# Performance work log

Measured on AMD Instinct MI355X. Metric: run time of the kernel, lower is better.

Reference implementation:

```python
import jax, jax.numpy as jnp
import numpy as np

D_MODEL = 1024
N_HEAD = 16
POWER = 4
EPS = 1e-6
MASK_FILL = -1000.0


def setup_inputs() -> dict:
    key = jax.random.key(0)
    ks = jax.random.split(key, 10)
    B, T, C = 2, 2048, D_MODEL
    sc = 1.0 / np.sqrt(C)
    inp = {
        "x": jax.random.normal(ks[0], (B, T, C), jnp.float32),
        "Wq": jax.random.normal(ks[1], (C, C), jnp.float32) * sc,
        "bq": jnp.zeros((C,), jnp.float32),
        "Wk": jax.random.normal(ks[2], (C, C), jnp.float32) * sc,
        "bk": jnp.zeros((C,), jnp.float32),
        "Wv": jax.random.normal(ks[3], (C, C), jnp.float32) * sc,
        "bv": jnp.zeros((C,), jnp.float32),
        "Wo": jax.random.normal(ks[4], (C, C), jnp.float32) * sc,
        "bo": jnp.zeros((C,), jnp.float32),
        "score_gain": jnp.asarray(4.0, jnp.float32),
        # True above the diagonal -> masked (causal)
        "causal_mask": jnp.triu(jnp.ones((T, T), jnp.bool_), k=1),
    }
    return inp


def rational_softmax(x):
    s = x / (jnp.abs(x) + 1.0)          # squash to (-1, 1)
    p = ((s + 1.0) * 0.5) ** POWER      # (0,1) then sharpen
    return p / (jnp.sum(p, axis=-1, keepdims=True) + EPS)


def reference(x, Wq, bq, Wk, bk, Wv, bv, Wo, bo, score_gain, causal_mask):
    B, T, C = x.shape
    H, D = N_HEAD, C // N_HEAD
    q = (x @ Wq + bq).reshape(B, T, H, D)
    k = (x @ Wk + bk).reshape(B, T, H, D)
    v = (x @ Wv + bv).reshape(B, T, H, D)
    # scores: (B, H, T, T)
    scores = jnp.einsum('bqhd,bkhd->bhqk', q, k)
    scores = scores - jnp.mean(scores, axis=-1, keepdims=True)
    mad = jnp.mean(jnp.abs(scores), axis=-1, keepdims=True) + 1e-6
    scores = scores / mad * score_gain
    scores = jnp.where(causal_mask, MASK_FILL, scores)
    attn = rational_softmax(scores)
    out = jnp.einsum('bhqk,bkhd->bqhd', attn, v).reshape(B, T, C)
    return out @ Wo + bo
```

## Files before the change

kernel.cpp:

```cpp
#include <hip/hip_runtime.h>
#include <hip/hip_bf16.h>
#include <cstdint>

#define BDIM 2
#define TSEQ 2048
#define CDIM 1024
#define NH 16
#define HD 64
#define NTOK (BDIM*TSEQ)
#define MASK_FILL_V (-1000.0f)
#define EPS_V (1e-6f)

typedef short bf16x8 __attribute__((ext_vector_type(8)));
typedef float f32x4  __attribute__((ext_vector_type(4)));

__device__ __forceinline__ float bf2f(unsigned short u) {
    union { unsigned int i; float f; } x; x.i = ((unsigned int)u) << 16; return x.f;
}
__device__ __forceinline__ unsigned short f2bf(float v) {
    __hip_bfloat16 h = __float2bfloat16(v);
    union { __hip_bfloat16 h; unsigned short u; } c; c.h = h; return c.u;
}
__device__ __forceinline__ float unpk_lo(unsigned int u) {
    union { unsigned int i; float f; } x; x.i = u << 16; return x.f;
}
__device__ __forceinline__ float unpk_hi(unsigned int u) {
    union { unsigned int i; float f; } x; x.i = u & 0xFFFF0000u; return x.f;
}
__device__ __forceinline__ unsigned int pk2(float lo, float hi) {
    unsigned int r;
    asm("v_cvt_pk_bf16_f32 %0, %1, %2" : "=v"(r) : "v"(lo), "v"(hi));
    return r;
}

__device__ __forceinline__ bool dt_is_bf16(const void* gain_p) {
    return ((*(const unsigned int*)gain_p) & 0xFFFFu) == 0x4080u;
}
__device__ __forceinline__ float ld1(const void* p, size_t i, bool bf) {
    return bf ? bf2f(((const unsigned short*)p)[i]) : ((const float*)p)[i];
}

__device__ __forceinline__ void gl2lds16(const unsigned short* g, unsigned short* l) {
    __builtin_amdgcn_global_load_lds(
        (const __attribute__((address_space(1))) unsigned int*)g,
        (__attribute__((address_space(3))) unsigned int*)l, 16, 0, 0);
}

__global__ __launch_bounds__(256) void pack_x_kernel(
    const void* __restrict__ X, const void* __restrict__ gain_p,
    unsigned short* __restrict__ Xb)
{
    const bool bf = dt_is_bf16(gain_p);
    size_t i = ((size_t)blockIdx.x * 256 + threadIdx.x) * 8;
    if (bf) {
        *(bf16x8*)&Xb[i] = *(const bf16x8*)((const unsigned short*)X + i);
    } else {
        const float* xf = (const float*)X;
        float4 a = *(const float4*)&xf[i];
        float4 b = *(const float4*)&xf[i + 4];
        bf16x8 o;
        o[0]=(short)f2bf(a.x); o[1]=(short)f2bf(a.y); o[2]=(short)f2bf(a.z); o[3]=(short)f2bf(a.w);
        o[4]=(short)f2bf(b.x); o[5]=(short)f2bf(b.y); o[6]=(short)f2bf(b.z); o[7]=(short)f2bf(b.w);
        *(bf16x8*)&Xb[i] = o;
    }
}

__global__ __launch_bounds__(256) void pack_wt_kernel(
    const void* __restrict__ Wq, const void* __restrict__ Wk,
    const void* __restrict__ Wv, const void* __restrict__ Wo,
    const void* __restrict__ gain_p, unsigned short* __restrict__ Wt)
{
    __shared__ __align__(16) unsigned short tile[64][72];
    const bool bf = dt_is_bf16(gain_p);
    const int which = blockIdx.z;
    const void* W = (which == 0) ? Wq : (which == 1) ? Wk : (which == 2) ? Wv : Wo;
    const int k0 = blockIdx.y * 64, n0 = blockIdx.x * 64;
    const int t = threadIdx.x;
    const int r = t >> 2, cb = (t & 3) * 16;
    if (bf) {
        const unsigned short* wsd = (const unsigned short*)W;
        *(bf16x8*)&tile[r][cb]     = *(const bf16x8*)&wsd[(size_t)(k0 + r) * CDIM + n0 + cb];
        *(bf16x8*)&tile[r][cb + 8] = *(const bf16x8*)&wsd[(size_t)(k0 + r) * CDIM + n0 + cb + 8];
    } else {
        const float* wf = (const float*)W;
        const float* src = &wf[(size_t)(k0 + r) * CDIM + n0 + cb];
        float4 f0 = *(const float4*)&src[0];
        float4 f1 = *(const float4*)&src[4];
        float4 f2 = *(const float4*)&src[8];
        float4 f3 = *(const float4*)&src[12];
        bf16x8 o0, o1;
        o0[0]=(short)f2bf(f0.x); o0[1]=(short)f2bf(f0.y); o0[2]=(short)f2bf(f0.z); o0[3]=(short)f2bf(f0.w);
        o0[4]=(short)f2bf(f1.x); o0[5]=(short)f2bf(f1.y); o0[6]=(short)f2bf(f1.z); o0[7]=(short)f2bf(f1.w);
        o1[0]=(short)f2bf(f2.x); o1[1]=(short)f2bf(f2.y); o1[2]=(short)f2bf(f2.z); o1[3]=(short)f2bf(f2.w);
        o1[4]=(short)f2bf(f3.x); o1[5]=(short)f2bf(f3.y); o1[6]=(short)f2bf(f3.z); o1[7]=(short)f2bf(f3.w);
        *(bf16x8*)&tile[r][cb]     = o0;
        *(bf16x8*)&tile[r][cb + 8] = o1;
    }
    __syncthreads();
    const int dr = t >> 2, tb = (t & 3) * 16;
    __align__(16) unsigned short tmp[16];
#pragma unroll
    for (int j = 0; j < 16; ++j) tmp[j] = tile[tb + j][dr];
    unsigned short* dst = Wt + ((size_t)(which * CDIM + n0 + dr)) * CDIM + k0 + tb;
    *(bf16x8*)&dst[0] = *(bf16x8*)&tmp[0];
    *(bf16x8*)&dst[8] = *(bf16x8*)&tmp[8];
}

__global__ __launch_bounds__(256) void gemm_mfma_kernel(
    const unsigned short* __restrict__ A,
    const unsigned short* __restrict__ Bt,
    const void* __restrict__ b0p, const void* __restrict__ b1p,
    const void* __restrict__ b2p,
    const void* __restrict__ gain_p,
    unsigned short* __restrict__ qkv,
    void* __restrict__ outp, int mode)
{
    __shared__ __align__(16) unsigned short As[128 * 32];
    __shared__ __align__(16) unsigned short Bs[128 * 32];

    const bool bf = dt_is_bf16(gain_p);
    const int t = threadIdx.x;
    const int w = t >> 6, lane = t & 63, quad = lane >> 4, l16 = lane & 15;
    const int wm = w >> 1, wn = w & 1;
    const int n0 = blockIdx.x * 128, m0 = blockIdx.y * 128;

    const unsigned short* Ag = A  + (size_t)m0 * CDIM;
    const unsigned short* Bg = Bt + (size_t)n0 * CDIM;

    f32x4 acc[4][4];
#pragma unroll
    for (int mt = 0; mt < 4; ++mt)
#pragma unroll
        for (int nt = 0; nt < 4; ++nt)
            acc[mt][nt] = (f32x4){0.f, 0.f, 0.f, 0.f};

    for (int kt = 0; kt < CDIM / 32; ++kt) {
        const int k0 = kt * 32;
#pragma unroll
        for (int i = 0; i < 2; ++i) {
            const int chunk = (i * 4 + w) * 64 + lane;
            const int row = chunk >> 2, kp = (chunk & 3) * 8;
            gl2lds16(Ag + (size_t)row * CDIM + k0 + kp, &As[(i * 4 + w) * 512]);
            gl2lds16(Bg + (size_t)row * CDIM + k0 + kp, &Bs[(i * 4 + w) * 512]);
        }
        __syncthreads();
        bf16x8 af[4], bfr[4];
#pragma unroll
        for (int mt = 0; mt < 4; ++mt)
            af[mt] = *(const bf16x8*)&As[(wm * 64 + mt * 16 + l16) * 32 + quad * 8];
#pragma unroll
        for (int nt = 0; nt < 4; ++nt)
            bfr[nt] = *(const bf16x8*)&Bs[(wn * 64 + nt * 16 + l16) * 32 + quad * 8];
#pragma unroll
        for (int mt = 0; mt < 4; ++mt)
#pragma unroll
            for (int nt = 0; nt < 4; ++nt)
                acc[mt][nt] = __builtin_amdgcn_mfma_f32_16x16x32_bf16(af[mt], bfr[nt], acc[mt][nt], 0, 0, 0);
        __syncthreads();
    }

    if (mode == 0) {
        const int which = n0 >> 10;
        if (which < 2) {
            const void* biasP = (which == 0) ? b0p : b1p;
            unsigned short* out = qkv + (size_t)which * NTOK * CDIM;
#pragma unroll
            for (int nt = 0; nt < 4; ++nt) {
                const int np = (n0 & 1023) + wn * 64 + nt * 16 + l16;
                const int h = np >> 6, d = np & 63;
                const float bias = ld1(biasP, np, bf);
#pragma unroll
                for (int mt = 0; mt < 4; ++mt)
#pragma unroll
                    for (int r = 0; r < 4; ++r) {
                        const int m = m0 + wm * 64 + mt * 16 + quad * 4 + r;
                        const int bb = m >> 11, tt = m & (TSEQ - 1);
                        out[(((size_t)(bb * NH + h)) * TSEQ + tt) * HD + d] =
                            f2bf(acc[mt][nt][r] + bias);
                    }
            }
        } else {
            unsigned short* vt = (unsigned short*)outp;
#pragma unroll
            for (int nt = 0; nt < 4; ++nt) {
                const int np = (n0 & 1023) + wn * 64 + nt * 16 + l16;
                const int h = np >> 6, d = np & 63;
                const float bias = ld1(b2p, np, bf);
#pragma unroll
                for (int mt = 0; mt < 4; ++mt) {
                    const int m = m0 + wm * 64 + mt * 16 + quad * 4;
                    const int bb = m >> 11, tt0 = m & (TSEQ - 1);
                    unsigned int lo = ((unsigned int)f2bf(acc[mt][nt][1] + bias) << 16)
                                    |  (unsigned int)f2bf(acc[mt][nt][0] + bias);
                    unsigned int hi = ((unsigned int)f2bf(acc[mt][nt][3] + bias) << 16)
                                    |  (unsigned int)f2bf(acc[mt][nt][2] + bias);
                    uint2 pk; pk.x = lo; pk.y = hi;
                    *(uint2*)&vt[((size_t)(bb * NH + h) * HD + d) * TSEQ + tt0] = pk;
                }
            }
        }
    } else {
#pragma unroll
        for (int nt = 0; nt < 4; ++nt) {
            const int np = n0 + wn * 64 + nt * 16 + l16;
            const float bias = ld1(b0p, np, bf);
#pragma unroll
            for (int mt = 0; mt < 4; ++mt)
#pragma unroll
                for (int r = 0; r < 4; ++r) {
                    const int m = m0 + wm * 64 + mt * 16 + quad * 4 + r;
                    const float v = acc[mt][nt][r] + bias;
                    if (bf) ((__hip_bfloat16*)outp)[(size_t)m * CDIM + np] = __float2bfloat16(v);
                    else    ((float*)outp)[(size_t)m * CDIM + np] = v;
                }
        }
    }
}

__global__ __launch_bounds__(256) void ksum_kernel(
    const unsigned short* __restrict__ Kb, float* __restrict__ Ksum)
{
    __shared__ float red[32][64];
    const int bh = blockIdx.x;
    const int t = threadIdx.x;
    const int d8 = (t & 7) * 8, g = t >> 3;
    const unsigned short* kp = Kb + (size_t)bh * TSEQ * HD;
    float s[8] = {};
    for (int tt = g; tt < TSEQ; tt += 32) {
        bf16x8 v = *(const bf16x8*)&kp[(size_t)tt * HD + d8];
#pragma unroll
        for (int j = 0; j < 8; ++j) s[j] += bf2f((unsigned short)v[j]);
    }
#pragma unroll
    for (int j = 0; j < 8; ++j) red[g][d8 + j] = s[j];
    __syncthreads();
    if (t < 64) {
        float tot = 0.f;
#pragma unroll
        for (int gg = 0; gg < 32; ++gg) tot += red[gg][t];
        Ksum[(size_t)bh * HD + t] = tot;
    }
}

#define QROWS 16
#define NQT (TSEQ / QROWS)

__global__ __launch_bounds__(512, 4) void attn_mfma_kernel(
    const unsigned short* __restrict__ Qb,
    const unsigned short* __restrict__ Kb,
    const unsigned short* __restrict__ Vt,
    const float* __restrict__ Ksum,
    const void* __restrict__ gain_p,
    unsigned short* __restrict__ AOb)
{
    __shared__ float smad[8][16];
    __shared__ float spsum[8][16];
    __shared__ float pvp[8][16 * 68];

    const bool bf = dt_is_bf16(gain_p);
    const float gain = ld1(gain_p, 0, bf);

    const int t    = threadIdx.x;
    const int w    = t >> 6;
    const int lane = t & 63;
    const int quad = lane >> 4;
    const int l16  = lane & 15;
    const int b4   = quad & 1, b5 = quad >> 1;

    const int id = blockIdx.x;
    const int bh = id & 31;
    const int q0 = (NQT - 1 - (id >> 5)) * QROWS;
    const int b  = bh >> 4, h = bh & 15;
    const size_t base = (size_t)bh * TSEQ * HD;

    bf16x8 qf[2];
    qf[0] = *(const bf16x8*)&Qb[base + (size_t)(q0 + l16) * HD + quad * 8];
    qf[1] = *(const bf16x8*)&Qb[base + (size_t)(q0 + l16) * HD + 32 + quad * 8];

    const float* Ks = Ksum + (size_t)bh * HD;
    float4 kA0 = *(const float4*)&Ks[quad * 8];
    float4 kA1 = *(const float4*)&Ks[quad * 8 + 4];
    float4 kB0 = *(const float4*)&Ks[32 + quad * 8];
    float4 kB1 = *(const float4*)&Ks[32 + quad * 8 + 4];
    float m;
    m  = bf2f((unsigned short)qf[0][0]) * kA0.x;
    m  = fmaf(bf2f((unsigned short)qf[0][1]), kA0.y, m);
    m  = fmaf(bf2f((unsigned short)qf[0][2]), kA0.z, m);
    m  = fmaf(bf2f((unsigned short)qf[0][3]), kA0.w, m);
    m  = fmaf(bf2f((unsigned short)qf[0][4]), kA1.x, m);
    m  = fmaf(bf2f((unsigned short)qf[0][5]), kA1.y, m);
    m  = fmaf(bf2f((unsigned short)qf[0][6]), kA1.z, m);
    m  = fmaf(bf2f((unsigned short)qf[0][7]), kA1.w, m);
    m  = fmaf(bf2f((unsigned short)qf[1][0]), kB0.x, m);
    m  = fmaf(bf2f((unsigned short)qf[1][1]), kB0.y, m);
    m  = fmaf(bf2f((unsigned short)qf[1][2]), kB0.z, m);
    m  = fmaf(bf2f((unsigned short)qf[1][3]), kB0.w, m);
    m  = fmaf(bf2f((unsigned short)qf[1][4]), kB1.x, m);
    m  = fmaf(bf2f((unsigned short)qf[1][5]), kB1.y, m);
    m  = fmaf(bf2f((unsigned short)qf[1][6]), kB1.z, m);
    m  = fmaf(bf2f((unsigned short)qf[1][7]), kB1.w, m);
    m += __shfl_xor(m, 16);
    m += __shfl_xor(m, 32);
    const float mean = m * (1.0f / TSEQ);

    const unsigned short* kp = Kb + base + (size_t)(w * 16 + l16) * HD + quad * 8;
    bf16x8 kbuf[2][2];
    kbuf[0][0] = *(const bf16x8*)&kp[0];
    kbuf[0][1] = *(const bf16x8*)&kp[32];
    kbuf[1][0] = *(const bf16x8*)&kp[8192];
    kbuf[1][1] = *(const bf16x8*)&kp[8192 + 32];

    unsigned int pkw[16][2];
    float madp = 0.f;
#pragma unroll
    for (int i = 0; i < 16; ++i) {
        bf16x8 c0 = kbuf[i & 1][0], c1 = kbuf[i & 1][1];
        if (i + 2 < 16) {
            kbuf[i & 1][0] = *(const bf16x8*)&kp[(size_t)(i + 2) * 8192];
            kbuf[i & 1][1] = *(const bf16x8*)&kp[(size_t)(i + 2) * 8192 + 32];
        }
        f32x4 s = (f32x4){0.f, 0.f, 0.f, 0.f};
        s = __builtin_amdgcn_mfma_f32_16x16x32_bf16(c0, qf[0], s, 0, 0, 0);
        s = __builtin_amdgcn_mfma_f32_16x16x32_bf16(c1, qf[1], s, 0, 0, 0);
        float d0 = s[0] - mean, d1 = s[1] - mean;
        float d2 = s[2] - mean, d3 = s[3] - mean;
        madp += fabsf(d0) + fabsf(d1);
        madp += fabsf(d2) + fabsf(d3);
        pkw[i][0] = pk2(d0, d1);
        pkw[i][1] = pk2(d2, d3);
    }
    madp += __shfl_xor(madp, 16);
    madp += __shfl_xor(madp, 32);
    if (lane < 16) smad[w][lane] = madp;
    __syncthreads();

    float msum = 0.f;
#pragma unroll
    for (int ww = 0; ww < 8; ++ww) msum += smad[ww][l16];
    const float scale = gain / (msum * (1.0f / TSEQ) + 1e-6f);

    const int NTmax = q0 >> 4;
    const int dif   = NTmax - w;
    const int i_max = (dif >= 0) ? (dif >> 3) : -1;

    const bool kgt0 = (quad * 4 + 0) > l16;
    const bool kgt1 = (quad * 4 + 1) > l16;
    const bool kgt2 = (quad * 4 + 2) > l16;
    const bool kgt3 = (quad * 4 + 3) > l16;

    float psum = 0.f;
    f32x4 acc0 = (f32x4){0.f,0.f,0.f,0.f};
    f32x4 acc1 = (f32x4){0.f,0.f,0.f,0.f};
    f32x4 acc2 = (f32x4){0.f,0.f,0.f,0.f};
    f32x4 acc3 = (f32x4){0.f,0.f,0.f,0.f};

    auto rsoft = [](float vv) -> float {
        float rc = __builtin_amdgcn_rcpf(fabsf(vv) + 1.0f);
        float ss = vv * rc;
        float u  = fmaf(ss, 0.5f, 0.5f);
        float u2 = u * u;
        return u2 * u2;
    };
    auto xform = [&](unsigned int plo, unsigned int phi, bool mask,
                     unsigned int& P0, unsigned int& P1) {
        float v0 = unpk_lo(plo) * scale, v1 = unpk_hi(plo) * scale;
        float v2 = unpk_lo(phi) * scale, v3 = unpk_hi(phi) * scale;
        if (mask) {
            if (kgt0) v0 = MASK_FILL_V;
            if (kgt1) v1 = MASK_FILL_V;
            if (kgt2) v2 = MASK_FILL_V;
            if (kgt3) v3 = MASK_FILL_V;
        }
        float p0 = rsoft(v0), p1 = rsoft(v1), p2 = rsoft(v2), p3 = rsoft(v3);
        psum += (p0 + p1) + (p2 + p3);
        P0 = pk2(p0, p1);
        P1 = pk2(p2, p3);
    };

    const unsigned short* vp = Vt + ((size_t)bh * HD + l16) * TSEQ
                               + w * 16 + b5 * 128 + b4 * 8;
#pragma unroll
    for (int j = 0; j < 8; ++j) {
        if (2 * j <= i_max) {
            unsigned int A0, A1, B0, B1;
            xform(pkw[2 * j][0], pkw[2 * j][1], (w + 16 * j) == NTmax, A0, A1);
            if (2 * j + 1 <= i_max) {
                xform(pkw[2 * j + 1][0], pkw[2 * j + 1][1],
                      (w + 16 * j + 8) == NTmax, B0, B1);
            } else { B0 = 0u; B1 = 0u; }
            unsigned int K0 = b5 ? B0 : A0, K1 = b5 ? B1 : A1;
            unsigned int T0 = b5 ? A0 : B0, T1 = b5 ? A1 : B1;
            unsigned int R0 = (unsigned int)__shfl_xor((int)T0, 32);
            unsigned int R1 = (unsigned int)__shfl_xor((int)T1, 32);
            unsigned int S0 = (b5 ^ b4) ? K0 : R0, S1 = (b5 ^ b4) ? K1 : R1;
            unsigned int U0 = (unsigned int)__shfl_xor((int)S0, 16);
            unsigned int U1 = (unsigned int)__shfl_xor((int)S1, 16);
            union { unsigned int u[4]; bf16x8 v; } fr;
            fr.u[0] = b4 ? U0 : (b5 ? R0 : K0);
            fr.u[1] = b4 ? U1 : (b5 ? R1 : K1);
            fr.u[2] = b4 ? (b5 ? K0 : R0) : U0;
            fr.u[3] = b4 ? (b5 ? K1 : R1) : U1;

            bf16x8 vb0 = *(const bf16x8*)&vp[j * 256 + 0 * 32768];
            bf16x8 vb1 = *(const bf16x8*)&vp[j * 256 + 1 * 32768];
            bf16x8 vb2 = *(const bf16x8*)&vp[j * 256 + 2 * 32768];
            bf16x8 vb3 = *(const bf16x8*)&vp[j * 256 + 3 * 32768];
            acc0 = __builtin_amdgcn_mfma_f32_16x16x32_bf16(fr.v, vb0, acc0, 0, 0, 0);
            acc1 = __builtin_amdgcn_mfma_f32_16x16x32_bf16(fr.v, vb1, acc1, 0, 0, 0);
            acc2 = __builtin_amdgcn_mfma_f32_16x16x32_bf16(fr.v, vb2, acc2, 0, 0, 0);
            acc3 = __builtin_amdgcn_mfma_f32_16x16x32_bf16(fr.v, vb3, acc3, 0, 0, 0);
        }
    }

    psum += __shfl_xor(psum, 16);
    psum += __shfl_xor(psum, 32);
    if (lane < 16) spsum[w][lane] = psum;

#pragma unroll
    for (int r = 0; r < 4; ++r) {
        const int qi = quad * 4 + r;
        pvp[w][qi * 68 +      l16] = acc0[r];
        pvp[w][qi * 68 + 16 + l16] = acc1[r];
        pvp[w][qi * 68 + 32 + l16] = acc2[r];
        pvp[w][qi * 68 + 48 + l16] = acc3[r];
    }
    __syncthreads();

    {
        const int q  = t >> 5;
        const int d2 = (t & 31) * 2;
        float s0 = 0.f, s1 = 0.f;
#pragma unroll
        for (int ww = 0; ww < 8; ++ww) {
            const float* pp = &pvp[ww][q * 68 + d2];
            s0 += pp[0];
            s1 += pp[1];
        }
        float ps = 0.f;
#pragma unroll
        for (int ww = 0; ww < 8; ++ww) ps += spsum[ww][q];
        const float inv = 1.0f / (ps + EPS_V);
        unsigned int o = ((unsigned int)f2bf(s1 * inv) << 16) | (unsigned int)f2bf(s0 * inv);
        *(unsigned int*)&AOb[((size_t)(b * TSEQ + q0 + q)) * CDIM + h * HD + d2] = o;
    }
}

extern "C" void kernel_launch(void* const* d_in, const int* in_sizes, int n_in,
                              void* d_out, int out_size, void* d_ws, size_t ws_size,
                              hipStream_t stream)
{
    (void)in_sizes; (void)n_in; (void)out_size; (void)ws_size;
    const void* X    = d_in[0];
    const void* Wq   = d_in[1];
    const void* bq   = d_in[2];
    const void* Wk   = d_in[3];
    const void* bk   = d_in[4];
    const void* Wv   = d_in[5];
    const void* bv   = d_in[6];
    const void* Wo   = d_in[7];
    const void* bo   = d_in[8];
    const void* gain = d_in[9];

    char* ws = (char*)d_ws;
    unsigned short* Xb  = (unsigned short*)ws;
    unsigned short* Wt  = (unsigned short*)(ws + (8ull  << 20));
    unsigned short* QKV = (unsigned short*)(ws + (16ull << 20));
    unsigned short* Vt  = (unsigned short*)(ws + (40ull << 20));
    unsigned short* AOb = (unsigned short*)(ws + (48ull << 20));
    float*          Ks  = (float*)(ws + (56ull << 20));
    unsigned short* Qb  = QKV;
    unsigned short* Kb  = QKV + (size_t)NTOK * CDIM;

    pack_x_kernel<<<NTOK * CDIM / (256 * 8), 256, 0, stream>>>(X, gain, Xb);
    pack_wt_kernel<<<dim3(16, 16, 4), 256, 0, stream>>>(Wq, Wk, Wv, Wo, gain, Wt);

    dim3 g1(3 * CDIM / 128, NTOK / 128);
    gemm_mfma_kernel<<<g1, 256, 0, stream>>>(Xb, Wt, bq, bk, bv, gain, QKV, Vt, 0);

    ksum_kernel<<<BDIM * NH, 256, 0, stream>>>(Kb, Ks);

    attn_mfma_kernel<<<(TSEQ / QROWS) * BDIM * NH, 512, 0, stream>>>(
        Qb, Kb, Vt, Ks, gain, AOb);

    dim3 g3(CDIM / 128, NTOK / 128);
    gemm_mfma_kernel<<<g3, 256, 0, stream>>>(AOb, Wt + 3ull * CDIM * CDIM, bo, bo, bo, gain,
                                             nullptr, d_out, 1);
}
```

Measured before the change: 385.2 us.

## Pair causal query tiles per block to share K loads and balance work

Each attention block now handles two 16-row query tiles, one early and one late in the causal order, so the K-tile loads and MFMA operands are shared across both score computations and every block does a similar amount of work. The grid is halved and the launch bound drops to 2 blocks per CU to make room for the doubled packed-score register arrays. The cost is higher register pressure and lower occupancy, and the two PV phases run one after the other with an extra barrier.

```diff
diff --git a/kernel.cpp b/kernel.cpp
--- a/kernel.cpp
+++ b/kernel.cpp
@@ -245,7 +245,7 @@
 #define QROWS 16
 #define NQT (TSEQ / QROWS)
 
-__global__ __launch_bounds__(512, 4) void attn_mfma_kernel(
+__global__ __launch_bounds__(512, 2) void attn_mfma_kernel(
     const unsigned short* __restrict__ Qb,
     const unsigned short* __restrict__ Kb,
     const unsigned short* __restrict__ Vt,
@@ -253,8 +253,8 @@
     const void* __restrict__ gain_p,
     unsigned short* __restrict__ AOb)
 {
-    __shared__ float smad[8][16];
-    __shared__ float spsum[8][16];
+    __shared__ float smad[2][8][16];
+    __shared__ float spsum[2][8][16];
     __shared__ float pvp[8][16 * 68];
 
     const bool bf = dt_is_bf16(gain_p);
@@ -269,39 +269,47 @@
 
     const int id = blockIdx.x;
     const int bh = id & 31;
-    const int q0 = (NQT - 1 - (id >> 5)) * QROWS;
+    const int p  = id >> 5;
+    const int q0a = p * QROWS;
+    const int q0b = (NQT - 1 - p) * QROWS;
     const int b  = bh >> 4, h = bh & 15;
     const size_t base = (size_t)bh * TSEQ * HD;
 
-    bf16x8 qf[2];
-    qf[0] = *(const bf16x8*)&Qb[base + (size_t)(q0 + l16) * HD + quad * 8];
-    qf[1] = *(const bf16x8*)&Qb[base + (size_t)(q0 + l16) * HD + 32 + quad * 8];
+    bf16x8 qfA[2], qfB[2];
+    qfA[0] = *(const bf16x8*)&Qb[base + (size_t)(q0a + l16) * HD + quad * 8];
+    qfA[1] = *(const bf16x8*)&Qb[base + (size_t)(q0a + l16) * HD + 32 + quad * 8];
+    qfB[0] = *(const bf16x8*)&Qb[base + (size_t)(q0b + l16) * HD + quad * 8];
+    qfB[1] = *(const bf16x8*)&Qb[base + (size_t)(q0b + l16) * HD + 32 + quad * 8];
 
     const float* Ks = Ksum + (size_t)bh * HD;
     float4 kA0 = *(const float4*)&Ks[quad * 8];
     float4 kA1 = *(const float4*)&Ks[quad * 8 + 4];
     float4 kB0 = *(const float4*)&Ks[32 + quad * 8];
     float4 kB1 = *(const float4*)&Ks[32 + quad * 8 + 4];
-    float m;
-    m  = bf2f((unsigned short)qf[0][0]) * kA0.x;
-    m  = fmaf(bf2f((unsigned short)qf[0][1]), kA0.y, m);
-    m  = fmaf(bf2f((unsigned short)qf[0][2]), kA0.z, m);
-    m  = fmaf(bf2f((unsigned short)qf[0][3]), kA0.w, m);
-    m  = fmaf(bf2f((unsigned short)qf[0][4]), kA1.x, m);
-    m  = fmaf(bf2f((unsigned short)qf[0][5]), kA1.y, m);
-    m  = fmaf(bf2f((unsigned short)qf[0][6]), kA1.z, m);
-    m  = fmaf(bf2f((unsigned short)qf[0][7]), kA1.w, m);
-    m  = fmaf(bf2f((unsigned short)qf[1][0]), kB0.x, m);
-    m  = fmaf(bf2f((unsigned short)qf[1][1]), kB0.y, m);
-    m  = fmaf(bf2f((unsigned short)qf[1][2]), kB0.z, m);
-    m  = fmaf(bf2f((unsigned short)qf[1][3]), kB0.w, m);
-    m  = fmaf(bf2f((unsigned short)qf[1][4]), kB1.x, m);
-    m  = fmaf(bf2f((unsigned short)qf[1][5]), kB1.y, m);
-    m  = fmaf(bf2f((unsigned short)qf[1][6]), kB1.z, m);
-    m  = fmaf(bf2f((unsigned short)qf[1][7]), kB1.w, m);
-    m += __shfl_xor(m, 16);
-    m += __shfl_xor(m, 32);
-    const float mean = m * (1.0f / TSEQ);
+    auto qdot = [&](const bf16x8 (&qf)[2]) -> float {
+        float m;
+        m  = bf2f((unsigned short)qf[0][0]) * kA0.x;
+        m  = fmaf(bf2f((unsigned short)qf[0][1]), kA0.y, m);
+        m  = fmaf(bf2f((unsigned short)qf[0][2]), kA0.z, m);
+        m  = fmaf(bf2f((unsigned short)qf[0][3]), kA0.w, m);
+        m  = fmaf(bf2f((unsigned short)qf[0][4]), kA1.x, m);
+        m  = fmaf(bf2f((unsigned short)qf[0][5]), kA1.y, m);
+        m  = fmaf(bf2f((unsigned short)qf[0][6]), kA1.z, m);
+        m  = fmaf(bf2f((unsigned short)qf[0][7]), kA1.w, m);
+        m  = fmaf(bf2f((unsigned short)qf[1][0]), kB0.x, m);
+        m  = fmaf(bf2f((unsigned short)qf[1][1]), kB0.y, m);
+        m  = fmaf(bf2f((unsigned short)qf[1][2]), kB0.z, m);
+        m  = fmaf(bf2f((unsigned short)qf[1][3]), kB0.w, m);
+        m  = fmaf(bf2f((unsigned short)qf[1][4]), kB1.x, m);
+        m  = fmaf(bf2f((unsigned short)qf[1][5]), kB1.y, m);
+        m  = fmaf(bf2f((unsigned short)qf[1][6]), kB1.z, m);
+        m  = fmaf(bf2f((unsigned short)qf[1][7]), kB1.w, m);
+        m += __shfl_xor(m, 16);
+        m += __shfl_xor(m, 32);
+        return m * (1.0f / TSEQ);
+    };
+    const float meanA = qdot(qfA);
+    const float meanB = qdot(qfB);
 
     const unsigned short* kp = Kb + base + (size_t)(w * 16 + l16) * HD + quad * 8;
     bf16x8 kbuf[2][2];
@@ -310,8 +318,8 @@
     kbuf[1][0] = *(const bf16x8*)&kp[8192];
     kbuf[1][1] = *(const bf16x8*)&kp[8192 + 32];
 
-    unsigned int pkw[16][2];
-    float madp = 0.f;
+    unsigned int pkwA[16][2], pkwB[16][2];
+    float madpA = 0.f, madpB = 0.f;
 #pragma unroll
     for (int i = 0; i < 16; ++i) {
         bf16x8 c0 = kbuf[i & 1][0], c1 = kbuf[i & 1][1];
@@ -319,40 +327,51 @@
             kbuf[i & 1][0] = *(const bf16x8*)&kp[(size_t)(i + 2) * 8192];
             kbuf[i & 1][1] = *(const bf16x8*)&kp[(size_t)(i + 2) * 8192 + 32];
         }
-        f32x4 s = (f32x4){0.f, 0.f, 0.f, 0.f};
-        s = __builtin_amdgcn_mfma_f32_16x16x32_bf16(c0, qf[0], s, 0, 0, 0);
-        s = __builtin_amdgcn_mfma_f32_16x16x32_bf16(c1, qf[1], s, 0, 0, 0);
-        float d0 = s[0] - mean, d1 = s[1] - mean;
-        float d2 = s[2] - mean, d3 = s[3] - mean;
-        madp += fabsf(d0) + fabsf(d1);
-        madp += fabsf(d2) + fabsf(d3);
-        pkw[i][0] = pk2(d0, d1);
-        pkw[i][1] = pk2(d2, d3);
-    }
-    madp += __shfl_xor(madp, 16);
-    madp += __shfl_xor(madp, 32);
-    if (lane < 16) smad[w][lane] = madp;
+        f32x4 sA = (f32x4){0.f, 0.f, 0.f, 0.f};
+        f32x4 sB = (f32x4){0.f, 0.f, 0.f, 0.f};
+        sA = __builtin_amdgcn_mfma_f32_16x16x32_bf16(c0, qfA[0], sA, 0, 0, 0);
+        sA = __builtin_amdgcn_mfma_f32_16x16x32_bf16(c1, qfA[1], sA, 0, 0, 0);
+        sB = __builtin_amdgcn_mfma_f32_16x16x32_bf16(c0, qfB[0], sB, 0, 0, 0);
+        sB = __builtin_amdgcn_mfma_f32_16x16x32_bf16(c1, qfB[1], sB, 0, 0, 0);
+        float a0 = sA[0] - meanA, a1 = sA[1] - meanA;
+        float a2 = sA[2] - meanA, a3 = sA[3] - meanA;
+        madpA += fabsf(a0) + fabsf(a1);
+        madpA += fabsf(a2) + fabsf(a3);
+        pkwA[i][0] = pk2(a0, a1);
+        pkwA[i][1] = pk2(a2, a3);
+        float e0 = sB[0] - meanB, e1 = sB[1] - meanB;
+        float e2 = sB[2] - meanB, e3 = sB[3] - meanB;
+        madpB += fabsf(e0) + fabsf(e1);
+        madpB += fabsf(e2) + fabsf(e3);
+        pkwB[i][0] = pk2(e0, e1);
+        pkwB[i][1] = pk2(e2, e3);
+    }
+    madpA += __shfl_xor(madpA, 16);
+    madpA += __shfl_xor(madpA, 32);
+    madpB += __shfl_xor(madpB, 16);
+    madpB += __shfl_xor(madpB, 32);
+    if (lane < 16) { smad[0][w][lane] = madpA; smad[1][w][lane] = madpB; }
     __syncthreads();
 
-    float msum = 0.f;
-#pragma unroll
-    for (int ww = 0; ww < 8; ++ww) msum += smad[ww][l16];
-    const float scale = gain / (msum * (1.0f / TSEQ) + 1e-6f);
-
-    const int NTmax = q0 >> 4;
-    const int dif   = NTmax - w;
-    const int i_max = (dif >= 0) ? (dif >> 3) : -1;
+    float msA = 0.f, msB = 0.f;
+#pragma unroll
+    for (int ww = 0; ww < 8; ++ww) { msA += smad[0][ww][l16]; msB += smad[1][ww][l16]; }
+    const float scaleA = gain / (msA * (1.0f / TSEQ) + 1e-6f);
+    const float scaleB = gain / (msB * (1.0f / TSEQ) + 1e-6f);
+
+    const int NTmaxA = p;
+    const int NTmaxB = NQT - 1 - p;
+    const int difA = NTmaxA - w;
+    const int i_maxA = (difA >= 0) ? (difA >> 3) : -1;
+    const int jmaxA  = (i_maxA >= 0) ? (i_maxA >> 1) : -1;
+    const int difB = NTmaxB - w;
+    const int i_maxB = (difB >= 0) ? (difB >> 3) : -1;
+    const int jmaxB  = (i_maxB >= 0) ? (i_maxB >> 1) : -1;
 
     const bool kgt0 = (quad * 4 + 0) > l16;
     const bool kgt1 = (quad * 4 + 1) > l16;
     const bool kgt2 = (quad * 4 + 2) > l16;
     const bool kgt3 = (quad * 4 + 3) > l16;
-
-    float psum = 0.f;
-    f32x4 acc0 = (f32x4){0.f,0.f,0.f,0.f};
-    f32x4 acc1 = (f32x4){0.f,0.f,0.f,0.f};
-    f32x4 acc2 = (f32x4){0.f,0.f,0.f,0.f};
-    f32x4 acc3 = (f32x4){0.f,0.f,0.f,0.f};
 
     auto rsoft = [](float vv) -> float {
         float rc = __builtin_amdgcn_rcpf(fabsf(vv) + 1.0f);
@@ -361,8 +380,8 @@
         float u2 = u * u;
         return u2 * u2;
     };
-    auto xform = [&](unsigned int plo, unsigned int phi, bool mask,
-                     unsigned int& P0, unsigned int& P1) {
+    auto xform = [&](unsigned int plo, unsigned int phi, bool mask, float scale,
+                     float& psum, unsigned int& P0, unsigned int& P1) {
         float v0 = unpk_lo(plo) * scale, v1 = unpk_hi(plo) * scale;
         float v2 = unpk_lo(phi) * scale, v3 = unpk_hi(phi) * scale;
         if (mask) {
@@ -376,56 +395,67 @@
         P0 = pk2(p0, p1);
         P1 = pk2(p2, p3);
     };
+    auto exch = [&](const unsigned int (&pk0)[2], const unsigned int (&pk1)[2],
+                    bool use1, bool mask0, bool mask1, float scale,
+                    float& psum, unsigned int (&fru)[4]) {
+        unsigned int A0, A1, B0, B1;
+        xform(pk0[0], pk0[1], mask0, scale, psum, A0, A1);
+        if (use1) xform(pk1[0], pk1[1], mask1, scale, psum, B0, B1);
+        else { B0 = 0u; B1 = 0u; }
+        unsigned int K0 = b5 ? B0 : A0, K1 = b5 ? B1 : A1;
+        unsigned int T0 = b5 ? A0 : B0, T1 = b5 ? A1 : B1;
+        unsigned int R0 = (unsigned int)__shfl_xor((int)T0, 32);
+        unsigned int R1 = (unsigned int)__shfl_xor((int)T1, 32);
+        unsigned int S0 = (b5 ^ b4) ? K0 : R0, S1 = (b5 ^ b4) ? K1 : R1;
+        unsigned int U0 = (unsigned int)__shfl_xor((int)S0, 16);
+        unsigned int U1 = (unsigned int)__shfl_xor((int)S1, 16);
+        fru[0] = b4 ? U0 : (b5 ? R0 : K0);
+        fru[1] = b4 ? U1 : (b5 ? R1 : K1);
+        fru[2] = b4 ? (b5 ? K0 : R0) : U0;
+        fru[3] = b4 ? (b5 ? K1 : R1) : U1;
+    };
 
     const unsigned short* vp = Vt + ((size_t)bh * HD + l16) * TSEQ
                                + w * 16 + b5 * 128 + b4 * 8;
-#pragma unroll
-    for (int j = 0; j < 8; ++j) {
-        if (2 * j <= i_max) {
-            unsigned int A0, A1, B0, B1;
-            xform(pkw[2 * j][0], pkw[2 * j][1], (w + 16 * j) == NTmax, A0, A1);
-            if (2 * j + 1 <= i_max) {
-                xform(pkw[2 * j + 1][0], pkw[2 * j + 1][1],
-                      (w + 16 * j + 8) == NTmax, B0, B1);
-            } else { B0 = 0u; B1 = 0u; }
-            unsigned int K0 = b5 ? B0 : A0, K1 = b5 ? B1 : A1;
-            unsigned int T0 = b5 ? A0 : B0, T1 = b5 ? A1 : B1;
-            unsigned int R0 = (unsigned int)__shfl_xor((int)T0, 32);
-            unsigned int R1 = (unsigned int)__shfl_xor((int)T1, 32);
-            unsigned int S0 = (b5 ^ b4) ? K0 : R0, S1 = (b5 ^ b4) ? K1 : R1;
-            unsigned int U0 = (unsigned int)__shfl_xor((int)S0, 16);
-            unsigned int U1 = (unsigned int)__shfl_xor((int)S1, 16);
-            union { unsigned int u[4]; bf16x8 v; } fr;
-            fr.u[0] = b4 ? U0 : (b5 ? R0 : K0);
-            fr.u[1] = b4 ? U1 : (b5 ? R1 : K1);
-            fr.u[2] = b4 ? (b5 ? K0 : R0) : U0;
-            fr.u[3] = b4 ? (b5 ? K1 : R1) : U1;
-
-            bf16x8 vb0 = *(const bf16x8*)&vp[j * 256 + 0 * 32768];
-            bf16x8 vb1 = *(const bf16x8*)&vp[j * 256 + 1 * 32768];
-            bf16x8 vb2 = *(const bf16x8*)&vp[j * 256 + 2 * 32768];
-            bf16x8 vb3 = *(const bf16x8*)&vp[j * 256 + 3 * 32768];
-            acc0 = __builtin_amdgcn_mfma_f32_16x16x32_bf16(fr.v, vb0, acc0, 0, 0, 0);
-            acc1 = __builtin_amdgcn_mfma_f32_16x16x32_bf16(fr.v, vb1, acc1, 0, 0, 0);
-            acc2 = __builtin_amdgcn_mfma_f32_16x16x32_bf16(fr.v, vb2, acc2, 0, 0, 0);
-            acc3 = __builtin_amdgcn_mfma_f32_16x16x32_bf16(fr.v, vb3, acc3, 0, 0, 0);
-        }
-    }
-
-    psum += __shfl_xor(psum, 16);
-    psum += __shfl_xor(psum, 32);
-    if (lane < 16) spsum[w][lane] = psum;
-
-#pragma unroll
-    for (int r = 0; r < 4; ++r) {
-        const int qi = quad * 4 + r;
-        pvp[w][qi * 68 +      l16] = acc0[r];
-        pvp[w][qi * 68 + 16 + l16] = acc1[r];
-        pvp[w][qi * 68 + 32 + l16] = acc2[r];
-        pvp[w][qi * 68 + 48 + l16] = acc3[r];
+
+    {
+        float psum = 0.f;
+        f32x4 acc0 = (f32x4){0.f,0.f,0.f,0.f};
+        f32x4 acc1 = (f32x4){0.f,0.f,0.f,0.f};
+        f32x4 acc2 = (f32x4){0.f,0.f,0.f,0.f};
+        f32x4 acc3 = (f32x4){0.f,0.f,0.f,0.f};
+#pragma unroll
+        for (int j = 0; j < 8; ++j) {
+            if (j <= jmaxA) {
+                unsigned int fru[4];
+                exch(pkwA[2 * j], pkwA[2 * j + 1], (2 * j + 1) <= i_maxA,
+                     (w + 16 * j) == NTmaxA, (w + 16 * j + 8) == NTmaxA,
+                     scaleA, psum, fru);
+                union { unsigned int u[4]; bf16x8 v; } F;
+                F.u[0] = fru[0]; F.u[1] = fru[1]; F.u[2] = fru[2]; F.u[3] = fru[3];
+                bf16x8 vb0 = *(const bf16x8*)&vp[j * 256 + 0 * 32768];
+                bf16x8 vb1 = *(const bf16x8*)&vp[j * 256 + 1 * 32768];
+                bf16x8 vb2 = *(const bf16x8*)&vp[j * 256 + 2 * 32768];
+                bf16x8 vb3 = *(const bf16x8*)&vp[j * 256 + 3 * 32768];
+                acc0 = __builtin_amdgcn_mfma_f32_16x16x32_bf16(F.v, vb0, acc0, 0, 0, 0);
+                acc1 = __builtin_amdgcn_mfma_f32_16x16x32_bf16(F.v, vb1, acc1, 0, 0, 0);
+                acc2 = __builtin_amdgcn_mfma_f32_16x16x32_bf16(F.v, vb2, acc2, 0, 0, 0);
+                acc3 = __builtin_amdgcn_mfma_f32_16x16x32_bf16(F.v, vb3, acc3, 0, 0, 0);
+            }
+        }
+        psum += __shfl_xor(psum, 16);
+        psum += __shfl_xor(psum, 32);
+        if (lane < 16) spsum[0][w][lane] = psum;
+#pragma unroll
+        for (int r = 0; r < 4; ++r) {
+            const int qi = quad * 4 + r;
+            pvp[w][qi * 68 +      l16] = acc0[r];
+            pvp[w][qi * 68 + 16 + l16] = acc1[r];
+            pvp[w][qi * 68 + 32 + l16] = acc2[r];
+            pvp[w][qi * 68 + 48 + l16] = acc3[r];
+        }
     }
     __syncthreads();
-
     {
         const int q  = t >> 5;
         const int d2 = (t & 31) * 2;
@@ -438,10 +468,67 @@
         }
         float ps = 0.f;
 #pragma unroll
-        for (int ww = 0; ww < 8; ++ww) ps += spsum[ww][q];
+        for (int ww = 0; ww < 8; ++ww) ps += spsum[0][ww][q];
         const float inv = 1.0f / (ps + EPS_V);
         unsigned int o = ((unsigned int)f2bf(s1 * inv) << 16) | (unsigned int)f2bf(s0 * inv);
-        *(unsigned int*)&AOb[((size_t)(b * TSEQ + q0 + q)) * CDIM + h * HD + d2] = o;
+        *(unsigned int*)&AOb[((size_t)(b * TSEQ + q0a + q)) * CDIM + h * HD + d2] = o;
+    }
+    __syncthreads();
+
+    {
+        float psum = 0.f;
+        f32x4 acc0 = (f32x4){0.f,0.f,0.f,0.f};
+        f32x4 acc1 = (f32x4){0.f,0.f,0.f,0.f};
+        f32x4 acc2 = (f32x4){0.f,0.f,0.f,0.f};
+        f32x4 acc3 = (f32x4){0.f,0.f,0.f,0.f};
+#pragma unroll
+        for (int j = 0; j < 8; ++j) {
+            if (j <= jmaxB) {
+                unsigned int fru[4];
+                exch(pkwB[2 * j], pkwB[2 * j + 1], (2 * j + 1) <= i_maxB,
+                     (w + 16 * j) == NTmaxB, (w + 16 * j + 8) == NTmaxB,
+                     scaleB, psum, fru);
+                union { unsigned int u[4]; bf16x8 v; } F;
+                F.u[0] = fru[0]; F.u[1] = fru[1]; F.u[2] = fru[2]; F.u[3] = fru[3];
+                bf16x8 vb0 = *(const bf16x8*)&vp[j * 256 + 0 * 32768];
+                bf16x8 vb1 = *(const bf16x8*)&vp[j * 256 + 1 * 32768];
+                bf16x8 vb2 = *(const bf16x8*)&vp[j * 256 + 2 * 32768];
+                bf16x8 vb3 = *(const bf16x8*)&vp[j * 256 + 3 * 32768];
+                acc0 = __builtin_amdgcn_mfma_f32_16x16x32_bf16(F.v, vb0, acc0, 0, 0, 0);
+                acc1 = __builtin_amdgcn_mfma_f32_16x16x32_bf16(F.v, vb1, acc1, 0, 0, 0);
+                acc2 = __builtin_amdgcn_mfma_f32_16x16x32_bf16(F.v, vb2, acc2, 0, 0, 0);
+                acc3 = __builtin_amdgcn_mfma_f32_16x16x32_bf16(F.v, vb3, acc3, 0, 0, 0);
+            }
+        }
+        psum += __shfl_xor(psum, 16);
+        psum += __shfl_xor(psum, 32);
+        if (lane < 16) spsum[1][w][lane] = psum;
+#pragma unroll
+        for (int r = 0; r < 4; ++r) {
+            const int qi = quad * 4 + r;
+            pvp[w][qi * 68 +      l16] = acc0[r];
+            pvp[w][qi * 68 + 16 + l16] = acc1[r];
+            pvp[w][qi * 68 + 32 + l16] = acc2[r];
+            pvp[w][qi * 68 + 48 + l16] = acc3[r];
+        }
+    }
+    __syncthreads();
+    {
+        const int q  = t >> 5;
+        const int d2 = (t & 31) * 2;
+        float s0 = 0.f, s1 = 0.f;
+#pragma unroll
+        for (int ww = 0; ww < 8; ++ww) {
+            const float* pp = &pvp[ww][q * 68 + d2];
+            s0 += pp[0];
+            s1 += pp[1];
+        }
+        float ps = 0.f;
+#pragma unroll
+        for (int ww = 0; ww < 8; ++ww) ps += spsum[1][ww][q];
+        const float inv = 1.0f / (ps + EPS_V);
+        unsigned int o = ((unsigned int)f2bf(s1 * inv) << 16) | (unsigned int)f2bf(s0 * inv);
+        *(unsigned int*)&AOb[((size_t)(b * TSEQ + q0b + q)) * CDIM + h * HD + d2] = o;
     }
 }
 
@@ -479,7 +566,7 @@
 
     ksum_kernel<<<BDIM * NH, 256, 0, stream>>>(Kb, Ks);
 
-    attn_mfma_kernel<<<(TSEQ / QROWS) * BDIM * NH, 512, 0, stream>>>(
+    attn_mfma_kernel<<<(NQT / 2) * BDIM * NH, 512, 0, stream>>>(
         Qb, Kb, Vt, Ks, gain, AOb);
 
     dim3 g3(CDIM / 128, NTOK / 128);
```

Result: faster. 328.7 us (-14.7%).
